# Kernel tuning notes

Measured on AMD Instinct MI355X. Metric: run time of the kernel, lower is better.

The kernel has to match this reference:

```python
import jax, jax.numpy as jnp
import numpy as np

B, I, H = 16384, 512, 512


def _linear_params(key, out_dim, in_dim):
    kw, kb = jax.random.split(key)
    bound = 1.0 / np.sqrt(in_dim)
    W = jax.random.uniform(kw, (out_dim, in_dim), jnp.float32, -bound, bound)
    b = jax.random.uniform(kb, (out_dim,), jnp.float32, -bound, bound)
    return W, b


def setup_inputs() -> dict:
    key = jax.random.key(0)
    ks = jax.random.split(key, 12)
    x = jax.random.normal(ks[0], (B, I), jnp.float32)
    h_prev = jax.random.normal(ks[1], (B, H), jnp.float32)
    c_prev = jax.random.normal(ks[2], (B, H), jnp.float32)
    W_xi, b_xi = _linear_params(ks[3], H, I)
    W_hi, b_hi = _linear_params(ks[4], H, H)
    W_xf, b_xf = _linear_params(ks[5], H, I)
    W_hf, b_hf = _linear_params(ks[6], H, H)
    W_xc, b_xc = _linear_params(ks[7], H, I)
    W_hc, b_hc = _linear_params(ks[8], H, H)
    W_xo, b_xo = _linear_params(ks[9], H, I)
    W_ho, b_ho = _linear_params(ks[10], H, H)
    W_e, b_e = _linear_params(ks[11], H, I + H)
    return dict(x=x, h_prev=h_prev, c_prev=c_prev,
                W_xi=W_xi, b_xi=b_xi, W_hi=W_hi, b_hi=b_hi,
                W_xf=W_xf, b_xf=b_xf, W_hf=W_hf, b_hf=b_hf,
                W_xc=W_xc, b_xc=b_xc, W_hc=W_hc, b_hc=b_hc,
                W_xo=W_xo, b_xo=b_xo, W_ho=W_ho, b_ho=b_ho,
                W_e=W_e, b_e=b_e)


def reference(x, h_prev, c_prev,
              W_xi, b_xi, W_hi, b_hi,
              W_xf, b_xf, W_hf, b_hf,
              W_xc, b_xc, W_hc, b_hc,
              W_xo, b_xo, W_ho, b_ho,
              W_e, b_e):
    # Batch the 4 input-to-hidden projections into one GEMM and the 4
    # hidden-to-hidden projections into another (same math as 8 Linears).
    Wx = jnp.concatenate([W_xi, W_xf, W_xc, W_xo], axis=0)   # [4H, I]
    bx = jnp.concatenate([b_xi, b_xf, b_xc, b_xo], axis=0)   # [4H]
    Wh = jnp.concatenate([W_hi, W_hf, W_hc, W_ho], axis=0)   # [4H, H]
    bh = jnp.concatenate([b_hi, b_hf, b_hc, b_ho], axis=0)
    gates = (x @ Wx.T + bx) + (h_prev @ Wh.T + bh)            # [B, 4H]
    gi, gf, gc, go = jnp.split(gates, 4, axis=-1)
    i = jax.nn.sigmoid(gi)
    f = jax.nn.sigmoid(gf)
    g = jnp.tanh(gc)
    o = jax.nn.sigmoid(go)
    c = f * c_prev + i * g
    # exp gate: Linear on [x, h_prev] -> tanh -> exp; split W_e to avoid concat
    We_x, We_h = W_e[:, :x.shape[-1]], W_e[:, x.shape[-1]:]
    exp_factor = jnp.exp(jnp.tanh(x @ We_x.T + h_prev @ We_h.T + b_e))
    h = o * jnp.tanh(c) * exp_factor
    return (h, c)
```

## Files before the change

kernel.cpp:

```cpp
#include <hip/hip_runtime.h>
#include <stdint.h>

#define Bsz 16384
#define Hh  512
#define Kd  1024
#define BM  128
#define BNJ 32
#define BK  32
#define NT  32

#define BBASE 24576

typedef __attribute__((ext_vector_type(8))) short bf16x8;
typedef __attribute__((ext_vector_type(4))) float f32x4;
typedef __attribute__((ext_vector_type(8))) unsigned short u16x8;

__device__ __forceinline__ unsigned short f2bf(float f) {
    union { float f; unsigned u; } v; v.f = f;
    unsigned u = v.u;
    return (unsigned short)((u + 0x7fffu + ((u >> 16) & 1u)) >> 16);
}
__device__ __forceinline__ float fast_tanh(float x) {
    float e = __expf(2.f * x);
    return (e - 1.f) / (e + 1.f);
}
__device__ __forceinline__ float fast_sigmoid(float x) {
    return 1.f / (1.f + __expf(-x));
}

__global__ void pack_A(const float* __restrict__ x, const float* __restrict__ h,
                       unsigned short* __restrict__ A) {
    const long total = (long)Bsz * Kd / 8;
    for (long i = (long)blockIdx.x * blockDim.x + threadIdx.x; i < total;
         i += (long)gridDim.x * blockDim.x) {
        long row = i >> 7;
        int  col = ((int)(i & 127)) << 3;
        const float* src = (col < 512) ? (x + row * 512 + col)
                                       : (h + row * 512 + (col - 512));
        float4 f0 = *(const float4*)(src);
        float4 f1 = *(const float4*)(src + 4);
        u16x8 o;
        o[0]=f2bf(f0.x); o[1]=f2bf(f0.y); o[2]=f2bf(f0.z); o[3]=f2bf(f0.w);
        o[4]=f2bf(f1.x); o[5]=f2bf(f1.y); o[6]=f2bf(f1.z); o[7]=f2bf(f1.w);
        *(u16x8*)(A + (i << 3)) = o;
    }
}

__global__ void pack_B(const float* __restrict__ Wxi, const float* __restrict__ Whi,
                       const float* __restrict__ Wxf, const float* __restrict__ Whf,
                       const float* __restrict__ Wxc, const float* __restrict__ Whc,
                       const float* __restrict__ Wxo, const float* __restrict__ Who,
                       const float* __restrict__ We,
                       const float* __restrict__ bxi, const float* __restrict__ bhi,
                       const float* __restrict__ bxf, const float* __restrict__ bhf,
                       const float* __restrict__ bxc, const float* __restrict__ bhc,
                       const float* __restrict__ bxo, const float* __restrict__ bho,
                       const float* __restrict__ be,
                       unsigned short* __restrict__ Bp, float* __restrict__ bias) {
    const long id = (long)blockIdx.x * blockDim.x + threadIdx.x;
    if (id < 327680) {
        int blk = (int)(id >> 6);
        int l   = (int)(id & 63);
        int kh  = blk & 1;
        int kt  = (blk >> 1) & 15;
        int rest = blk >> 5;
        int g    = rest % 5;
        int jgrp = rest / 5;
        int j  = jgrp * 16 + (l & 15);
        int k0 = kt * 64 + kh * 32 + ((l >> 4) << 3);
        const float* src;
        if (g == 4) {
            src = We + (long)j * 1024 + k0;
        } else {
            const float* Wx = (g == 0) ? Wxi : (g == 1) ? Wxf : (g == 2) ? Wxc : Wxo;
            const float* Wh = (g == 0) ? Whi : (g == 1) ? Whf : (g == 2) ? Whc : Who;
            src = (k0 < 512) ? (Wx + (long)j * 512 + k0)
                             : (Wh + (long)j * 512 + (k0 - 512));
        }
        float4 f0 = *(const float4*)(src);
        float4 f1 = *(const float4*)(src + 4);
        u16x8 o;
        o[0]=f2bf(f0.x); o[1]=f2bf(f0.y); o[2]=f2bf(f0.z); o[3]=f2bf(f0.w);
        o[4]=f2bf(f1.x); o[5]=f2bf(f1.y); o[6]=f2bf(f1.z); o[7]=f2bf(f1.w);
        *(u16x8*)(Bp + (long)blk * 512 + l * 8) = o;
    }
    if (id < 2560) {
        int row = (int)id;
        int g = row >> 9, j = row & 511;
        float b;
        if (g == 4) b = be[j];
        else {
            const float* bx = (g == 0) ? bxi : (g == 1) ? bxf : (g == 2) ? bxc : bxo;
            const float* bh = (g == 0) ? bhi : (g == 1) ? bhf : (g == 2) ? bhc : bho;
            b = bx[j] + bh[j];
        }
        bias[row] = b;
    }
}

#define GL16(g, l) __builtin_amdgcn_global_load_lds( \
    (const __attribute__((address_space(1))) unsigned int*)(g), \
    (__attribute__((address_space(3))) unsigned int*)(l), 16, 0, 0)

#define VM_I(n)    asm volatile("s_waitcnt vmcnt(" #n ")" ::: "memory")
#define VM(n)      VM_I(n)
#define LGKM0()    asm volatile("s_waitcnt lgkmcnt(0)" ::: "memory")
#define BARRIER()  asm volatile("s_barrier" ::: "memory")
#define SCHED0()   __builtin_amdgcn_sched_barrier(0)

#define MF(a, b, c) __builtin_amdgcn_mfma_f32_16x16x32_bf16(a, b, c, 0, 0, 0)

#define RD9(ABO, BBO) do { \
    afA[0] = *(const bf16x8*)(aP + (ABO) + 0 * 1024); \
    afA[1] = *(const bf16x8*)(aP + (ABO) + 1 * 1024); \
    afA[2] = *(const bf16x8*)(aP + (ABO) + 2 * 1024); \
    afA[3] = *(const bf16x8*)(aP + (ABO) + 3 * 1024); \
    bq[0]  = *(const bf16x8*)(bP + (BBO) + 0 * 1024); \
    bq[1]  = *(const bf16x8*)(bP + (BBO) + 1 * 1024); \
    bq[2]  = *(const bf16x8*)(bP + (BBO) + 2 * 1024); \
    bq[3]  = *(const bf16x8*)(bP + (BBO) + 3 * 1024); \
    bq[4]  = *(const bf16x8*)(bP + (BBO) + 4 * 1024); \
} while (0)

#define MFMA20() do { \
    __builtin_amdgcn_s_setprio(1); \
    _Pragma("unroll") \
    for (int g_ = 0; g_ < 5; ++g_) { \
        acc[g_][0] = MF(afA[0], bq[g_], acc[g_][0]); \
        acc[g_][1] = MF(afA[1], bq[g_], acc[g_][1]); \
        acc[g_][2] = MF(afA[2], bq[g_], acc[g_][2]); \
        acc[g_][3] = MF(afA[3], bq[g_], acc[g_][3]); \
    } \
    __builtin_amdgcn_s_setprio(0); \
} while (0)

#define SGA2(SAO, T) do { \
    GL16(asg0 + (T) * 32, lds_raw + (SAO) + adst0); \
    GL16(asg1 + (T) * 32, lds_raw + (SAO) + adst1); \
} while (0)

#define SGB3(SBO, T) do { \
    GL16(bsg0 + (T) * 512, lds_raw + BBASE + (SBO) + bdo0); \
    GL16(bsg1 + (T) * 512, lds_raw + BBASE + (SBO) + bdo1); \
    GL16(bsg2 + (T) * 512, lds_raw + BBASE + (SBO) + bdo2); \
} while (0)

#define TILE(ABO, BBO, SAO, SBO, T, SA, SB, WN, SYNC) do { \
    RD9(ABO, BBO); \
    if (SB) SGB3(SBO, (T) + 1); \
    if (SA) SGA2(SAO, (T) + 2); \
    LGKM0(); SCHED0(); \
    MFMA20(); \
    if (SYNC) { VM(WN); BARRIER(); } \
} while (0)

__global__ __launch_bounds__(256, 3)
void xlstm_gemm(const unsigned short* __restrict__ A,
                const unsigned short* __restrict__ Bp,
                const float* __restrict__ bias,
                const float* __restrict__ c_prev,
                float* __restrict__ out) {
    __shared__ __align__(16) unsigned char lds_raw[45056];

    const int tid  = threadIdx.x;
    const int wid  = tid >> 6;
    const int lane = tid & 63;
    const int wm   = wid >> 1;
    const int wj   = wid & 1;
    const int fr   = lane & 15;
    const int q    = lane >> 4;

    const int orig = blockIdx.x;
    const int wg   = (orig & 7) * 256 + (orig >> 3);
    const int mblk = wg >> 4;
    const int jblk = wg & 15;
    const long brow = (long)mblk * BM;
    const int  bcol = jblk * BNJ;

    f32x4 acc[5][4];
#pragma unroll
    for (int g = 0; g < 5; ++g)
#pragma unroll
        for (int m = 0; m < 4; ++m)
#pragma unroll
            for (int r = 0; r < 4; ++r) acc[g][m][r] = 0.f;

    bf16x8 afA[4];
    bf16x8 bq[5];

    const unsigned char* aP = lds_raw + wm * 4096 + fr * 64
                              + ((q ^ ((fr >> 1) & 3)) << 4);
    const unsigned char* bP = lds_raw + BBASE + wj * 5120 + lane * 16;

    const int arow = tid >> 2;
    const unsigned short* asg0 = A + (brow + arow) * 1024L
                                   + (((tid & 3) ^ ((arow >> 1) & 3)) << 3);
    const unsigned short* asg1 = asg0 + 65536;
    const int adst0 = tid * 16;
    const int adst1 = tid * 16 + 4096;
    const unsigned short *bsg0, *bsg1, *bsg2;
    int bdo0, bdo1, bdo2;
#define BSTG_INIT(i) do { \
    int u_ = wid + 4 * (i); if (u_ >= 10) u_ -= 10; \
    int jl_ = u_ / 5; int g_ = u_ - 5 * jl_; \
    bsg##i = Bp + (long)(jblk * 2 + jl_) * 81920 + g_ * 16384 + lane * 8; \
    bdo##i = u_ * 1024 + lane * 16; \
} while (0)
    BSTG_INIT(0); BSTG_INIT(1); BSTG_INIT(2);
#undef BSTG_INIT

    SGB3(0, 0);
    SGA2(0, 0);
    SGA2(8192, 1);
    VM(2);
    BARRIER();

    for (int t = 0; t < 30; t += 6) {
        TILE(0,     0,     16384, 10240, t + 0, 1, 1, 2, 1);
        TILE(8192,  10240, 0,     0,     t + 1, 1, 1, 2, 1);
        TILE(16384, 0,     8192,  10240, t + 2, 1, 1, 2, 1);
        TILE(0,     10240, 16384, 0,     t + 3, 1, 1, 2, 1);
        TILE(8192,  0,     0,     10240, t + 4, 1, 1, 2, 1);
        TILE(16384, 10240, 8192,  0,     t + 5, 1, 1, 2, 1);
    }
    TILE(0,    0,     0, 10240, 30, 0, 1, 0, 1);
    TILE(8192, 10240, 0, 0,     31, 0, 0, 0, 0);

    const int j = bcol + wj * 16 + fr;
    const float bi_ = bias[j];
    const float bf_ = bias[512 + j];
    const float bc_ = bias[1024 + j];
    const float bo_ = bias[1536 + j];
    const float be_ = bias[2048 + j];
    const long mbase = brow + wm * 64 + (q << 2);
#pragma unroll
    for (int m = 0; m < 4; ++m) {
#pragma unroll
        for (int r = 0; r < 4; ++r) {
            long row = mbase + m * 16 + r;
            float gi = acc[0][m][r] + bi_;
            float gf = acc[1][m][r] + bf_;
            float gc = acc[2][m][r] + bc_;
            float go = acc[3][m][r] + bo_;
            float ge = acc[4][m][r] + be_;
            float iv = fast_sigmoid(gi);
            float fv = fast_sigmoid(gf);
            float gv = fast_tanh(gc);
            float ov = fast_sigmoid(go);
            float ef = __expf(fast_tanh(ge));
            float cp = c_prev[row * 512 + j];
            float cv = fv * cp + iv * gv;
            float hv = ov * fast_tanh(cv) * ef;
            out[row * 512 + j] = hv;
            out[(long)Bsz * 512 + row * 512 + j] = cv;
        }
    }
}

extern "C" void kernel_launch(void* const* d_in, const int* in_sizes, int n_in,
                              void* d_out, int out_size, void* d_ws, size_t ws_size,
                              hipStream_t stream) {
    const float* x      = (const float*)d_in[0];
    const float* h_prev = (const float*)d_in[1];
    const float* c_prev = (const float*)d_in[2];
    const float* Wxi = (const float*)d_in[3];
    const float* bxi = (const float*)d_in[4];
    const float* Whi = (const float*)d_in[5];
    const float* bhi = (const float*)d_in[6];
    const float* Wxf = (const float*)d_in[7];
    const float* bxf = (const float*)d_in[8];
    const float* Whf = (const float*)d_in[9];
    const float* bhf = (const float*)d_in[10];
    const float* Wxc = (const float*)d_in[11];
    const float* bxc = (const float*)d_in[12];
    const float* Whc = (const float*)d_in[13];
    const float* bhc = (const float*)d_in[14];
    const float* Wxo = (const float*)d_in[15];
    const float* bxo = (const float*)d_in[16];
    const float* Who = (const float*)d_in[17];
    const float* bho = (const float*)d_in[18];
    const float* We  = (const float*)d_in[19];
    const float* be  = (const float*)d_in[20];

    unsigned short* Abf  = (unsigned short*)d_ws;
    unsigned short* Bp   = (unsigned short*)((char*)d_ws + 33554432);
    float*          bias = (float*)((char*)d_ws + 33554432 + 5242880);

    pack_A<<<2048, 256, 0, stream>>>(x, h_prev, Abf);
    pack_B<<<1280, 256, 0, stream>>>(Wxi, Whi, Wxf, Whf, Wxc, Whc, Wxo, Who, We,
                                     bxi, bhi, bxf, bhf, bxc, bhc, bxo, bho, be,
                                     Bp, bias);
    xlstm_gemm<<<2048, 256, 0, stream>>>(Abf, Bp, bias, c_prev, (float*)d_out);
}
```

Before: 119.3 us.

## Load A fragments directly from global into registers using MFMA-ordered packing

The A operand is repacked by pack_A into an MFMA fragment-major layout, so each wave can load its A fragments straight from global memory into registers with global_load_dwordx4. This drops A staging through LDS and the matching LDS reads. LDS now holds only B, shrinking the allocation from 45056 to 20480 bytes, and the pipeline is reduced to a 2-stage register double buffer. The cost is more VGPRs and A loads that are no longer shared between the two waves with the same wm, so each A fragment is fetched from global twice. Latency hiding may also suffer because the waitcnt now covers the register loads.

Measured after the change: 118.5 us. Within noise of the previous version (-0.7%).

```diff
diff --git a/kernel.cpp b/kernel.cpp
--- a/kernel.cpp
+++ b/kernel.cpp
@@ -9,8 +9,6 @@
 #define BK  32
 #define NT  32
 
-#define BBASE 24576
-
 typedef __attribute__((ext_vector_type(8))) short bf16x8;
 typedef __attribute__((ext_vector_type(4))) float f32x4;
 typedef __attribute__((ext_vector_type(8))) unsigned short u16x8;
@@ -33,10 +31,15 @@
     const long total = (long)Bsz * Kd / 8;
     for (long i = (long)blockIdx.x * blockDim.x + threadIdx.x; i < total;
          i += (long)gridDim.x * blockDim.x) {
-        long row = i >> 7;
-        int  col = ((int)(i & 127)) << 3;
-        const float* src = (col < 512) ? (x + row * 512 + col)
-                                       : (h + row * 512 + (col - 512));
+        int  l    = (int)(i & 63);
+        long blk  = i >> 6;
+        int  u    = (int)(blk & 7);
+        int  t    = (int)((blk >> 3) & 31);
+        long mblk = blk >> 8;
+        long row  = mblk * 128 + u * 16 + (l & 15);
+        int  k0   = t * 32 + ((l >> 4) << 3);
+        const float* src = (k0 < 512) ? (x + row * 512 + k0)
+                                      : (h + row * 512 + (k0 - 512));
         float4 f0 = *(const float4*)(src);
         float4 f1 = *(const float4*)(src + 4);
         u16x8 o;
@@ -104,63 +107,58 @@
 
 #define VM_I(n)    asm volatile("s_waitcnt vmcnt(" #n ")" ::: "memory")
 #define VM(n)      VM_I(n)
-#define LGKM0()    asm volatile("s_waitcnt lgkmcnt(0)" ::: "memory")
 #define BARRIER()  asm volatile("s_barrier" ::: "memory")
-#define SCHED0()   __builtin_amdgcn_sched_barrier(0)
 
 #define MF(a, b, c) __builtin_amdgcn_mfma_f32_16x16x32_bf16(a, b, c, 0, 0, 0)
 
-#define RD9(ABO, BBO) do { \
-    afA[0] = *(const bf16x8*)(aP + (ABO) + 0 * 1024); \
-    afA[1] = *(const bf16x8*)(aP + (ABO) + 1 * 1024); \
-    afA[2] = *(const bf16x8*)(aP + (ABO) + 2 * 1024); \
-    afA[3] = *(const bf16x8*)(aP + (ABO) + 3 * 1024); \
-    bq[0]  = *(const bf16x8*)(bP + (BBO) + 0 * 1024); \
-    bq[1]  = *(const bf16x8*)(bP + (BBO) + 1 * 1024); \
-    bq[2]  = *(const bf16x8*)(bP + (BBO) + 2 * 1024); \
-    bq[3]  = *(const bf16x8*)(bP + (BBO) + 3 * 1024); \
-    bq[4]  = *(const bf16x8*)(bP + (BBO) + 4 * 1024); \
-} while (0)
-
-#define MFMA20() do { \
+#define RDB5(RBO) do { \
+    bq0 = *(const bf16x8*)(bRP + (RBO) + 0 * 1024); \
+    bq1 = *(const bf16x8*)(bRP + (RBO) + 1 * 1024); \
+    bq2 = *(const bf16x8*)(bRP + (RBO) + 2 * 1024); \
+    bq3 = *(const bf16x8*)(bRP + (RBO) + 3 * 1024); \
+    bq4 = *(const bf16x8*)(bRP + (RBO) + 4 * 1024); \
+} while (0)
+
+#define MF4(S, BQ, G) \
+    acc[G][0] = MF(a##S##0, BQ, acc[G][0]); \
+    acc[G][1] = MF(a##S##1, BQ, acc[G][1]); \
+    acc[G][2] = MF(a##S##2, BQ, acc[G][2]); \
+    acc[G][3] = MF(a##S##3, BQ, acc[G][3]);
+
+#define MFMA20(S) do { \
     __builtin_amdgcn_s_setprio(1); \
-    _Pragma("unroll") \
-    for (int g_ = 0; g_ < 5; ++g_) { \
-        acc[g_][0] = MF(afA[0], bq[g_], acc[g_][0]); \
-        acc[g_][1] = MF(afA[1], bq[g_], acc[g_][1]); \
-        acc[g_][2] = MF(afA[2], bq[g_], acc[g_][2]); \
-        acc[g_][3] = MF(afA[3], bq[g_], acc[g_][3]); \
-    } \
+    MF4(S, bq0, 0) MF4(S, bq1, 1) MF4(S, bq2, 2) MF4(S, bq3, 3) MF4(S, bq4, 4) \
     __builtin_amdgcn_s_setprio(0); \
 } while (0)
 
-#define SGA2(SAO, T) do { \
-    GL16(asg0 + (T) * 32, lds_raw + (SAO) + adst0); \
-    GL16(asg1 + (T) * 32, lds_raw + (SAO) + adst1); \
+#define LOADA4(S, T) do { \
+    asm volatile("global_load_dwordx4 %0, %1, off" : "=v"(a##S##0) : "v"(asrc + (T) * 4096L + 0 * 512)); \
+    asm volatile("global_load_dwordx4 %0, %1, off" : "=v"(a##S##1) : "v"(asrc + (T) * 4096L + 1 * 512)); \
+    asm volatile("global_load_dwordx4 %0, %1, off" : "=v"(a##S##2) : "v"(asrc + (T) * 4096L + 2 * 512)); \
+    asm volatile("global_load_dwordx4 %0, %1, off" : "=v"(a##S##3) : "v"(asrc + (T) * 4096L + 3 * 512)); \
 } while (0)
 
 #define SGB3(SBO, T) do { \
-    GL16(bsg0 + (T) * 512, lds_raw + BBASE + (SBO) + bdo0); \
-    GL16(bsg1 + (T) * 512, lds_raw + BBASE + (SBO) + bdo1); \
-    GL16(bsg2 + (T) * 512, lds_raw + BBASE + (SBO) + bdo2); \
-} while (0)
-
-#define TILE(ABO, BBO, SAO, SBO, T, SA, SB, WN, SYNC) do { \
-    RD9(ABO, BBO); \
-    if (SB) SGB3(SBO, (T) + 1); \
-    if (SA) SGA2(SAO, (T) + 2); \
-    LGKM0(); SCHED0(); \
-    MFMA20(); \
-    if (SYNC) { VM(WN); BARRIER(); } \
+    GL16(bsg0 + (T) * 512, lds_raw + (SBO) + bdo0); \
+    GL16(bsg1 + (T) * 512, lds_raw + (SBO) + bdo1); \
+    GL16(bsg2 + (T) * 512, lds_raw + (SBO) + bdo2); \
+} while (0)
+
+#define STEP(T, S, RBO, SBO) do { \
+    SGB3(SBO, (T) + 1); \
+    RDB5(RBO); \
+    MFMA20(S); \
+    LOADA4(S, (T) + 2); \
+    VM(4); BARRIER(); \
 } while (0)
 
 __global__ __launch_bounds__(256, 3)
-void xlstm_gemm(const unsigned short* __restrict__ A,
+void xlstm_gemm(const unsigned short* __restrict__ Apk,
                 const unsigned short* __restrict__ Bp,
                 const float* __restrict__ bias,
                 const float* __restrict__ c_prev,
                 float* __restrict__ out) {
-    __shared__ __align__(16) unsigned char lds_raw[45056];
+    __shared__ __align__(16) unsigned char lds_raw[20480];
 
     const int tid  = threadIdx.x;
     const int wid  = tid >> 6;
@@ -185,19 +183,14 @@
 #pragma unroll
             for (int r = 0; r < 4; ++r) acc[g][m][r] = 0.f;
 
-    bf16x8 afA[4];
-    bf16x8 bq[5];
-
-    const unsigned char* aP = lds_raw + wm * 4096 + fr * 64
-                              + ((q ^ ((fr >> 1) & 3)) << 4);
-    const unsigned char* bP = lds_raw + BBASE + wj * 5120 + lane * 16;
-
-    const int arow = tid >> 2;
-    const unsigned short* asg0 = A + (brow + arow) * 1024L
-                                   + (((tid & 3) ^ ((arow >> 1) & 3)) << 3);
-    const unsigned short* asg1 = asg0 + 65536;
-    const int adst0 = tid * 16;
-    const int adst1 = tid * 16 + 4096;
+    bf16x8 aP0, aP1, aP2, aP3;
+    bf16x8 aQ0, aQ1, aQ2, aQ3;
+    bf16x8 bq0, bq1, bq2, bq3, bq4;
+
+    const unsigned short* asrc = Apk + (long)mblk * 131072 + wm * 2048 + lane * 8;
+
+    const unsigned char* bRP = lds_raw + wj * 5120 + lane * 16;
+
     const unsigned short *bsg0, *bsg1, *bsg2;
     int bdo0, bdo1, bdo2;
 #define BSTG_INIT(i) do { \
@@ -210,21 +203,21 @@
 #undef BSTG_INIT
 
     SGB3(0, 0);
-    SGA2(0, 0);
-    SGA2(8192, 1);
-    VM(2);
+    LOADA4(P, 0);
+    LOADA4(Q, 1);
+    VM(4);
     BARRIER();
 
-    for (int t = 0; t < 30; t += 6) {
-        TILE(0,     0,     16384, 10240, t + 0, 1, 1, 2, 1);
-        TILE(8192,  10240, 0,     0,     t + 1, 1, 1, 2, 1);
-        TILE(16384, 0,     8192,  10240, t + 2, 1, 1, 2, 1);
-        TILE(0,     10240, 16384, 0,     t + 3, 1, 1, 2, 1);
-        TILE(8192,  0,     0,     10240, t + 4, 1, 1, 2, 1);
-        TILE(16384, 10240, 8192,  0,     t + 5, 1, 1, 2, 1);
-    }
-    TILE(0,    0,     0, 10240, 30, 0, 1, 0, 1);
-    TILE(8192, 10240, 0, 0,     31, 0, 0, 0, 0);
+    for (int t = 0; t < 30; t += 2) {
+        STEP(t,     P, 0,     10240);
+        STEP(t + 1, Q, 10240, 0);
+    }
+    SGB3(10240, 31);
+    RDB5(0);
+    MFMA20(P);
+    VM(0); BARRIER();
+    RDB5(10240);
+    MFMA20(Q);
 
     const int j = bcol + wj * 16 + fr;
     const float bi_ = bias[j];
```
